# Kernel optimization log

Hardware: AMD Instinct MI355X
Metric: run time of the kernel (lower is better)

## Reference

```python
import jax, jax.numpy as jnp
import numpy as np

# 8 corner offsets of the trilinear cell: (8, 3)
_OFFS = jnp.array([[i, j, k] for i in (0, 1) for j in (0, 1) for k in (0, 1)], dtype=jnp.int32)


def _gridding(cloud, R):
    """Trilinear scatter of points into an RxRxR occupancy-weight grid.

    cloud: (b, n, 3) with coords in [-0.5, 0.5] (already divided by scale).
    Returns (b, R, R, R) grid where each point adds trilinear weights to its
    8 neighboring cells (the GRNet gridding_distance forward kernel).
    """
    b, n, _ = cloud.shape
    v = (cloud + 0.5) * R                      # continuous voxel coords in [0, R)
    lower = jnp.floor(v)
    frac = v - lower                           # (b, n, 3) in [0, 1)
    lower = lower.astype(jnp.int32)
    nb = lower[:, :, None, :] + _OFFS[None, None]              # (b, n, 8, 3)
    # per-axis trilinear weight: (1 - frac) for the low corner, frac for the high
    w_d = jnp.where(_OFFS[None, None] == 0,
                    1.0 - frac[:, :, None, :], frac[:, :, None, :])  # (b, n, 8, 3)
    w = jnp.prod(w_d, axis=-1)                                  # (b, n, 8)
    valid = jnp.all((nb >= 0) & (nb < R), axis=-1)              # (b, n, 8)
    w = jnp.where(valid, w, 0.0)
    nbc = jnp.clip(nb, 0, R - 1)
    flat = (nbc[..., 0] * R + nbc[..., 1]) * R + nbc[..., 2]    # (b, n, 8)
    batch_off = jnp.arange(b, dtype=jnp.int32)[:, None, None] * (R * R * R)
    idx = (flat + batch_off).reshape(-1)
    grid = jnp.zeros((b * R * R * R,), cloud.dtype).at[idx].add(w.reshape(-1))
    return grid.reshape(b, R, R, R)


def setup_inputs() -> dict:
    key = jax.random.key(0)
    k1, k2 = jax.random.split(key)
    R = 128
    B, N1, N2 = 16, 65536, 65536
    # coords in [-(R-2)/2, (R-2)/2] so that after /scale they are inside (-0.5, 0.5)
    pred = (jax.random.uniform(k1, (B, N1, 3), jnp.float32) - 0.5) * (R - 2)
    gt = (jax.random.uniform(k2, (B, N2, 3), jnp.float32) - 0.5) * (R - 2)
    return {"pred_cloud": pred, "gt_cloud": gt, "scale": R}


def reference(pred_cloud, gt_cloud, scale):
    pred = pred_cloud / scale
    gt = gt_cloud / scale
    return _gridding(pred, scale), _gridding(gt, scale)
```

## Files before the change

### kernel.cpp

```cpp
#include <hip/hip_runtime.h>
#include <stdint.h>


constexpr int R    = 128;
constexpr int R3c  = R * R * R;
constexpr int BPG  = 256;
constexpr int NBLK = 512;
constexpr int BLKT = 512;
constexpr int MAXB = 128;

constexpr size_t WS_HIST = 0;
constexpr size_t WS_TOT  = 768u << 10;
constexpr size_t WS_BASE = 1u << 20;
constexpr size_t WS_QREC = 2u << 20;
constexpr size_t WS_REC  = 20u << 20;

typedef float f4v __attribute__((ext_vector_type(4)));

__device__ __forceinline__ uint32_t quant1(float p) {
    const float S = 16384.0f;
    const uint32_t QMAX = (126u << 14) | 16383u;
    float v = p + 64.0f;
    return min(__float2uint_rn(fmaxf(v, 0.0f) * S), QMAX);
}

__device__ __forceinline__ uint2 pack_rec(uint32_t xq, uint32_t yq, uint32_t zq) {
    return make_uint2(xq | (yq << 21), (yq >> 11) | (zq << 10));
}
__device__ __forceinline__ void unpack_rec(uint2 r, uint32_t& xq, uint32_t& yq, uint32_t& zq) {
    xq = r.x & 0x1FFFFFu;
    yq = (r.x >> 21) | ((r.y & 0x3FFu) << 11);
    zq = (r.y >> 10) & 0x1FFFFFu;
}

__device__ __forceinline__ void region_range(uint32_t xq, uint32_t yq, uint32_t zq,
                                             int& rx0, int& rx1, int& ry0, int& ry1,
                                             int& rz0, int& rz1)
{
    int ix = xq >> 14, iy = yq >> 14, iz = zq >> 14;
    rx0 = ix >> 4; rx1 = (ix + 1) >> 4;
    ry0 = iy >> 4; ry1 = (iy + 1) >> 4;
    rz0 = iz >> 5; rz1 = (iz + 1) >> 5;
}

__global__ __launch_bounds__(BLKT) void bin_hist_qrec(
    const float* __restrict__ pred, const float* __restrict__ gt,
    int total1, int P, int ppb,
    uint32_t* __restrict__ hist, uint2* __restrict__ qrec)
{
    __shared__ uint32_t h[BPG];
    if (threadIdx.x < BPG) h[threadIdx.x] = 0;
    __syncthreads();

    int s = blockIdx.x * ppb;
    if (s < P) {
        int e = min(s + ppb, P);
        bool isgt = (s >= total1);
        const float* src = isgt ? gt + (size_t)(s - total1) * 3
                                : pred + (size_t)s * 3;
        const float4* src4 = (const float4*)src;
        int ngrp = (e - s) >> 2;
        for (int g = threadIdx.x; g < ngrp; g += BLKT) {
            float4 a  = src4[g * 3 + 0];
            float4 b4 = src4[g * 3 + 1];
            float4 c4 = src4[g * 3 + 2];
            float xs[4] = {a.x, a.w, b4.z, c4.y};
            float ys[4] = {a.y, b4.x, b4.w, c4.z};
            float zs[4] = {a.z, b4.y, c4.x, c4.w};
            uint2 rec[4];
            #pragma unroll
            for (int q = 0; q < 4; ++q) {
                uint32_t xq = quant1(xs[q]), yq = quant1(ys[q]), zq = quant1(zs[q]);
                rec[q] = pack_rec(xq, yq, zq);
                int rx0, rx1, ry0, ry1, rz0, rz1;
                region_range(xq, yq, zq, rx0, rx1, ry0, ry1, rz0, rz1);
                for (int aa = rx0; aa <= rx1; ++aa)
                    for (int bb = ry0; bb <= ry1; ++bb)
                        for (int cc = rz0; cc <= rz1; ++cc)
                            atomicAdd(&h[(aa << 5) + (bb << 2) + cc], 1u);
            }
            uint4* q4 = (uint4*)(qrec + (size_t)s + (size_t)g * 4);
            q4[0] = make_uint4(rec[0].x, rec[0].y, rec[1].x, rec[1].y);
            q4[1] = make_uint4(rec[2].x, rec[2].y, rec[3].x, rec[3].y);
        }
    }
    __syncthreads();
    if (threadIdx.x < BPG)
        hist[(size_t)blockIdx.x * BPG + threadIdx.x] = h[threadIdx.x];
}

__global__ __launch_bounds__(256) void scan1(
    uint32_t* __restrict__ hist, uint32_t* __restrict__ tot,
    int B, int nb1, int bpg1, int bpg2, int NBINS)
{
    int j = blockIdx.x * 256 + threadIdx.x;
    if (j >= NBINS) return;
    int cb = j >> 8, l = j & 255;
    int first = (cb < B) ? cb * bpg1 : nb1 + (cb - B) * bpg2;
    int cnt   = (cb < B) ? bpg1 : bpg2;
    uint32_t run = 0;
    for (int k = 0; k < cnt; ++k) {
        size_t idx = (size_t)(first + k) * BPG + l;
        uint32_t t = hist[idx];
        hist[idx] = run;
        run += t;
    }
    tot[j] = run;
}

__global__ __launch_bounds__(256) void scan_base(
    const uint32_t* __restrict__ tot, uint32_t* __restrict__ base, int NBINS)
{
    __shared__ uint32_t part[256];
    int t = threadIdx.x;
    int chunk = NBINS / 256;
    uint32_t s = 0;
    for (int i = 0; i < chunk; ++i) s += tot[t * chunk + i];
    part[t] = s;
    __syncthreads();
    if (t == 0) {
        uint32_t run = 0;
        for (int i = 0; i < 256; ++i) { uint32_t v = part[i]; part[i] = run; run += v; }
    }
    __syncthreads();
    uint32_t run = part[t];
    for (int i = 0; i < chunk; ++i) {
        base[t * chunk + i] = run;
        run += tot[t * chunk + i];
    }
    if (t == 255) base[NBINS] = run;
}

__global__ __launch_bounds__(BLKT) void bin_scatter_qrec(
    const uint2* __restrict__ qrec,
    int total1, int P, int n1, int n2, int B, int ppb,
    const uint32_t* __restrict__ hist, const uint32_t* __restrict__ base,
    uint2* __restrict__ records)
{
    int s = blockIdx.x * ppb;
    if (s >= P) return;
    int cb = (s < total1) ? (s / n1) : (B + (s - total1) / n2);

    __shared__ uint32_t cur[BPG];
    if (threadIdx.x < BPG)
        cur[threadIdx.x] = base[cb * BPG + threadIdx.x] +
                           hist[(size_t)blockIdx.x * BPG + threadIdx.x];
    __syncthreads();

    int e = min(s + ppb, P);
    const uint4* qr4 = (const uint4*)(qrec + (size_t)s);
    int ngrp = (e - s) >> 2;
    for (int g = threadIdx.x; g < ngrp; g += BLKT) {
        uint4 q0 = qr4[2 * g];
        uint4 q1 = qr4[2 * g + 1];
        uint2 rec[4] = {make_uint2(q0.x, q0.y), make_uint2(q0.z, q0.w),
                        make_uint2(q1.x, q1.y), make_uint2(q1.z, q1.w)};
        #pragma unroll
        for (int q = 0; q < 4; ++q) {
            uint32_t xq, yq, zq;
            unpack_rec(rec[q], xq, yq, zq);
            int rx0, rx1, ry0, ry1, rz0, rz1;
            region_range(xq, yq, zq, rx0, rx1, ry0, ry1, rz0, rz1);
            for (int aa = rx0; aa <= rx1; ++aa)
                for (int b2 = ry0; b2 <= ry1; ++b2)
                    for (int cc = rz0; cc <= rz1; ++cc) {
                        uint32_t slot =
                            atomicAdd(&cur[(aa << 5) + (b2 << 2) + cc], 1u);
                        records[slot] = rec[q];
                    }
        }
    }
}

__global__ __launch_bounds__(256) void accum_kernel(
    const uint32_t* __restrict__ base, const uint2* __restrict__ records,
    float* __restrict__ out)
{
    __shared__ float tile[16 * 16 * 32];
    int bin = blockIdx.x;
    int cb = bin >> 8;
    int region = bin & 255;
    int rx = region >> 5, ry = (region >> 2) & 7, rz = region & 3;

    float4* t4 = (float4*)tile;
    for (int t = threadIdx.x; t < 2048; t += 256)
        t4[t] = make_float4(0.f, 0.f, 0.f, 0.f);
    __syncthreads();

    uint32_t s = base[bin], e = base[bin + 1];
    const float FQ = 6.103515625e-05f;
    for (uint32_t r = s + threadIdx.x; r < e; r += 256) {
        uint32_t xq, yq, zq;
        unpack_rec(records[r], xq, yq, zq);
        int ix = xq >> 14, iy = yq >> 14, iz = zq >> 14;
        float fx = (float)(xq & 16383u) * FQ;
        float fy = (float)(yq & 16383u) * FQ;
        float fz = (float)(zq & 16383u) * FQ;
        float wx[2] = {1.0f - fx, fx};
        float wy[2] = {1.0f - fy, fy};
        float wz[2] = {1.0f - fz, fz};
        #pragma unroll
        for (int dx = 0; dx < 2; ++dx) {
            int cx = ix + dx;
            if ((cx >> 4) != rx) continue;
            #pragma unroll
            for (int dy = 0; dy < 2; ++dy) {
                int cy = iy + dy;
                if ((cy >> 4) != ry) continue;
                float wxy = wx[dx] * wy[dy];
                #pragma unroll
                for (int dz = 0; dz < 2; ++dz) {
                    int cz = iz + dz;
                    if ((cz >> 5) != rz) continue;
                    atomicAdd(&tile[(((cx & 15) << 4) + (cy & 15)) * 32 + (cz & 31)],
                              wxy * wz[dz]);
                }
            }
        }
    }
    __syncthreads();

    float* gout = out + (size_t)cb * R3c;
    for (int w = threadIdx.x; w < 2048; w += 256) {
        int lin = w * 4;
        int lx = lin >> 9, rem = lin & 511, ly = rem >> 5, lz = rem & 31;
        int X = rx * 16 + lx, Y = ry * 16 + ly, Z = rz * 32 + lz;
        f4v v = ((const f4v*)tile)[w];
        __builtin_nontemporal_store(v, (f4v*)&gout[((size_t)X * R + Y) * R + Z]);
    }
}

__device__ __forceinline__ void point_math_f(float px, float py, float pz,
                                             int& ix, int& iy, int& iz,
                                             float& fx, float& fy, float& fz)
{
    const float inv = 1.0f / 128.0f;
    float vx = (px * inv + 0.5f) * 128.0f;
    float vy = (py * inv + 0.5f) * 128.0f;
    float vz = (pz * inv + 0.5f) * 128.0f;
    float lx = floorf(vx), ly = floorf(vy), lz = floorf(vz);
    fx = vx - lx; fy = vy - ly; fz = vz - lz;
    ix = min(max((int)lx, 0), R - 2);
    iy = min(max((int)ly, 0), R - 2);
    iz = min(max((int)lz, 0), R - 2);
}

__global__ __launch_bounds__(256) void gridding_scatter(
    const float* __restrict__ cloud, float* __restrict__ grid,
    int total_pts, int n_per_batch)
{
    int idx = blockIdx.x * blockDim.x + threadIdx.x;
    if (idx >= total_pts) return;
    int b = idx / n_per_batch;
    const float* p = cloud + (size_t)idx * 3;
    int ix, iy, iz; float fx, fy, fz;
    point_math_f(p[0], p[1], p[2], ix, iy, iz, fx, fy, fz);
    float wx[2] = {1.0f - fx, fx};
    float wy[2] = {1.0f - fy, fy};
    float wz[2] = {1.0f - fz, fz};
    float* gb = grid + (size_t)b * R3c;
    #pragma unroll
    for (int dx = 0; dx < 2; ++dx)
        #pragma unroll
        for (int dy = 0; dy < 2; ++dy) {
            float wxy = wx[dx] * wy[dy];
            #pragma unroll
            for (int dz = 0; dz < 2; ++dz)
                atomicAdd(gb + ((size_t)(ix + dx) * R + (iy + dy)) * R + (iz + dz),
                          wxy * wz[dz]);
        }
}

extern "C" void kernel_launch(void* const* d_in, const int* in_sizes, int n_in,
                              void* d_out, int out_size, void* d_ws, size_t ws_size,
                              hipStream_t stream) {
    const float* pred = (const float*)d_in[0];
    const float* gt   = (const float*)d_in[1];
    float* out = (float*)d_out;

    int total1 = in_sizes[0] / 3;
    int total2 = in_sizes[1] / 3;
    int B  = out_size / (2 * R3c);
    int n1 = total1 / B;
    int n2 = total2 / B;
    int NBINS = 2 * B * BPG;
    int P  = total1 + total2;
    int ppb = (P + NBLK - 1) / NBLK;

    bool fastok = (ppb % 4 == 0) && (n1 % ppb == 0) && (n2 % ppb == 0) &&
                  (n1 > 0) && (n2 > 0) && (B > 0) && (B <= MAXB) &&
                  (NBINS % 256 == 0) &&
                  (total1 % n1 == 0) && (total2 % n2 == 0);
    size_t ws_need = WS_REC + (size_t)8 * P * 8;
    if (!fastok || ws_size < ws_need) {
        hipMemsetAsync(d_out, 0, (size_t)out_size * sizeof(float), stream);
        gridding_scatter<<<(total1 + 255) / 256, 256, 0, stream>>>(pred, out, total1, n1);
        gridding_scatter<<<(total2 + 255) / 256, 256, 0, stream>>>(
            gt, out + (size_t)B * R3c, total2, n2);
        return;
    }

    uint32_t* hist  = (uint32_t*)((char*)d_ws + WS_HIST);
    uint32_t* tot   = (uint32_t*)((char*)d_ws + WS_TOT);
    uint32_t* basep = (uint32_t*)((char*)d_ws + WS_BASE);
    uint2*    qrec  = (uint2*)((char*)d_ws + WS_QREC);
    uint2*    recs  = (uint2*)((char*)d_ws + WS_REC);

    int nb1  = total1 / ppb;
    int bpg1 = n1 / ppb;
    int bpg2 = n2 / ppb;

    bin_hist_qrec<<<NBLK, BLKT, 0, stream>>>(pred, gt, total1, P, ppb, hist, qrec);
    scan1<<<(NBINS + 255) / 256, 256, 0, stream>>>(hist, tot, B, nb1, bpg1, bpg2, NBINS);
    scan_base<<<1, 256, 0, stream>>>(tot, basep, NBINS);
    bin_scatter_qrec<<<NBLK, BLKT, 0, stream>>>(qrec, total1, P, n1, n2, B, ppb,
                                                hist, basep, recs);
    accum_kernel<<<NBINS, 256, 0, stream>>>(basep, recs, out);
}
```

Baseline: 386.2 us.

## Fuse histogram, scans and bin scatter into one cooperative kernel

Replaces the four-kernel binning pipeline (histogram, per-bin scan, base scan, scatter) with one cooperative kernel that uses grid-wide syncs between phases. Each thread keeps its quantized records in registers, so the intermediate qrec buffer is neither written nor read back. This removes kernel launch gaps and that round trip through memory. In exchange it adds grid.sync barriers, caps occupancy through the launch bound, and leaves the middle scan phases running on only part of the grid.

```diff
diff --git a/kernel.cpp b/kernel.cpp
--- a/kernel.cpp
+++ b/kernel.cpp
@@ -1,6 +1,9 @@
 #include <hip/hip_runtime.h>
+#include <hip/hip_cooperative_groups.h>
 #include <stdint.h>
 
+
+namespace cg = cooperative_groups;
 
 constexpr int R    = 128;
 constexpr int R3c  = R * R * R;
@@ -42,6 +45,116 @@
     ry0 = iy >> 4; ry1 = (iy + 1) >> 4;
     rz0 = iz >> 5; rz1 = (iz + 1) >> 5;
 }
+
+__global__ __launch_bounds__(BLKT, 4) void fused_sort(
+    const float* __restrict__ pred, const float* __restrict__ gt,
+    int total1, int P, int ppb, int B, int nb1, int bpg1, int bpg2, int NBINS,
+    uint32_t* __restrict__ hist, uint32_t* __restrict__ tot,
+    uint32_t* __restrict__ base, uint2* __restrict__ records)
+{
+    __shared__ uint32_t shm[BLKT];
+    cg::grid_group grid = cg::this_grid();
+
+    if (threadIdx.x < BPG) shm[threadIdx.x] = 0;
+    __syncthreads();
+
+    int s = blockIdx.x * ppb;
+    bool isgt = (s >= total1);
+    const float4* src4 = (const float4*)(isgt ? gt + (size_t)(s - total1) * 3
+                                              : pred + (size_t)s * 3);
+    uint2 lrec[2][4];
+    #pragma unroll
+    for (int it = 0; it < 2; ++it) {
+        int g = threadIdx.x + it * BLKT;
+        float4 a  = src4[g * 3 + 0];
+        float4 b4 = src4[g * 3 + 1];
+        float4 c4 = src4[g * 3 + 2];
+        float xs[4] = {a.x, a.w, b4.z, c4.y};
+        float ys[4] = {a.y, b4.x, b4.w, c4.z};
+        float zs[4] = {a.z, b4.y, c4.x, c4.w};
+        #pragma unroll
+        for (int q = 0; q < 4; ++q) {
+            uint32_t xq = quant1(xs[q]), yq = quant1(ys[q]), zq = quant1(zs[q]);
+            lrec[it][q] = pack_rec(xq, yq, zq);
+            int rx0, rx1, ry0, ry1, rz0, rz1;
+            region_range(xq, yq, zq, rx0, rx1, ry0, ry1, rz0, rz1);
+            for (int aa = rx0; aa <= rx1; ++aa)
+                for (int bb = ry0; bb <= ry1; ++bb)
+                    for (int cc = rz0; cc <= rz1; ++cc)
+                        atomicAdd(&shm[(aa << 5) + (bb << 2) + cc], 1u);
+        }
+    }
+    __syncthreads();
+    if (threadIdx.x < BPG)
+        hist[(size_t)blockIdx.x * BPG + threadIdx.x] = shm[threadIdx.x];
+    __threadfence();
+    grid.sync();
+
+    int tid = blockIdx.x * BLKT + threadIdx.x;
+    if (tid < NBINS) {
+        int cb = tid >> 8, l = tid & 255;
+        int first = (cb < B) ? cb * bpg1 : nb1 + (cb - B) * bpg2;
+        int cnt   = (cb < B) ? bpg1 : bpg2;
+        uint32_t run = 0;
+        for (int k = 0; k < cnt; ++k) {
+            size_t idx = (size_t)(first + k) * BPG + l;
+            uint32_t t = hist[idx];
+            hist[idx] = run;
+            run += t;
+        }
+        tot[tid] = run;
+    }
+    __threadfence();
+    grid.sync();
+
+    if (blockIdx.x == 0) {
+        int t = threadIdx.x;
+        int chunk = NBINS / BLKT;
+        uint32_t ssum = 0;
+        for (int i = 0; i < chunk; ++i) ssum += tot[t * chunk + i];
+        shm[t] = ssum;
+        __syncthreads();
+        if (t == 0) {
+            uint32_t run = 0;
+            for (int i = 0; i < BLKT; ++i) { uint32_t v = shm[i]; shm[i] = run; run += v; }
+        }
+        __syncthreads();
+        uint32_t run = shm[t];
+        for (int i = 0; i < chunk; ++i) {
+            base[t * chunk + i] = run;
+            run += tot[t * chunk + i];
+        }
+        if (t == BLKT - 1) base[NBINS] = run;
+    }
+    __threadfence();
+    grid.sync();
+
+    int cbb = (blockIdx.x < nb1) ? (blockIdx.x / bpg1)
+                                 : (B + (blockIdx.x - nb1) / bpg2);
+    if (threadIdx.x < BPG)
+        shm[threadIdx.x] = base[cbb * BPG + threadIdx.x] +
+                           hist[(size_t)blockIdx.x * BPG + threadIdx.x];
+    __syncthreads();
+
+    #pragma unroll
+    for (int it = 0; it < 2; ++it) {
+        #pragma unroll
+        for (int q = 0; q < 4; ++q) {
+            uint2 rec = lrec[it][q];
+            uint32_t xq, yq, zq;
+            unpack_rec(rec, xq, yq, zq);
+            int rx0, rx1, ry0, ry1, rz0, rz1;
+            region_range(xq, yq, zq, rx0, rx1, ry0, ry1, rz0, rz1);
+            for (int aa = rx0; aa <= rx1; ++aa)
+                for (int bb = ry0; bb <= ry1; ++bb)
+                    for (int cc = rz0; cc <= rz1; ++cc) {
+                        uint32_t slot = atomicAdd(&shm[(aa << 5) + (bb << 2) + cc], 1u);
+                        records[slot] = rec;
+                    }
+        }
+    }
+}
+
 
 __global__ __launch_bounds__(BLKT) void bin_hist_qrec(
     const float* __restrict__ pred, const float* __restrict__ gt,
@@ -310,6 +423,23 @@
     int bpg1 = n1 / ppb;
     int bpg2 = n2 / ppb;
 
+    bool coopok = fastok && (ppb == 8 * BLKT) && (P == NBLK * ppb) &&
+                  (NBINS % BLKT == 0) && (NBINS <= NBLK * BLKT);
+    if (coopok) {
+        void* args[] = {(void*)&pred, (void*)&gt, (void*)&total1, (void*)&P,
+                        (void*)&ppb, (void*)&B, (void*)&nb1, (void*)&bpg1,
+                        (void*)&bpg2, (void*)&NBINS, (void*)&hist, (void*)&tot,
+                        (void*)&basep, (void*)&recs};
+        hipError_t err = hipLaunchCooperativeKernel(
+            reinterpret_cast<const void*>(&fused_sort),
+            dim3(NBLK), dim3(BLKT), args, 0, stream);
+        if (err == hipSuccess) {
+            accum_kernel<<<NBINS, 256, 0, stream>>>(basep, recs, out);
+            return;
+        }
+        (void)hipGetLastError();
+    }
+
     bin_hist_qrec<<<NBLK, BLKT, 0, stream>>>(pred, gt, total1, P, ppb, hist, qrec);
     scan1<<<(NBINS + 255) / 256, 256, 0, stream>>>(hist, tot, B, nb1, bpg1, bpg2, NBINS);
     scan_base<<<1, 256, 0, stream>>>(tot, basep, NBINS);
```

Result: slower. 689.2 us (+78.5%).
